# Kernel optimization log

Hardware: AMD Instinct MI355X
Metric: run time of the kernel (lower is better)

The kernel has to match this reference:

```python
import jax, jax.numpy as jnp
import numpy as np

B = 8192

def setup_inputs() -> dict:
    key = jax.random.key(0)
    k1, k2, k3 = jax.random.split(key, 3)
    pred = jax.random.normal(k1, (B,), dtype=jnp.float32)
    frac_time = jax.random.uniform(k2, (B,), dtype=jnp.float32) * 100.0
    if_mof = (jax.random.uniform(k3, (B,)) < 0.7).astype(jnp.float32)  # 0/1 flags
    gt = jnp.stack([frac_time, if_mof], axis=1)  # [B, 2]
    return {"pred": pred, "gt": gt, "gt_fracTime": 0, "gt_ifMOF": 1}


def reference(pred, gt, gt_fracTime, gt_ifMOF):
    # pred: [B], gt: [B,2]
    target = gt[:, gt_fracTime]          # [B]
    if_mof = gt[:, gt_ifMOF]             # [B], 0/1 flags
    flag = (if_mof == 1).astype(pred.dtype)
    n = pred.shape[0]
    # valid pairs: i < j with both flags set (loss term is symmetric in (i,j))
    triu = jnp.triu(jnp.ones((n, n), dtype=bool), k=1)
    pair_mask = (flag[:, None] * flag[None, :]) * triu.astype(pred.dtype)  # [B,B]
    dp = pred[:, None] - pred[None, :]      # [B,B]
    dt = target[:, None] - target[None, :]  # [B,B]
    loss = jnp.maximum(dp * dt / 100.0, 0.0)
    n_pairs = pair_mask.sum()
    return (loss * pair_mask).sum() / n_pairs
```

## Files before the change

kernel.cpp:

```cpp
#include <hip/hip_runtime.h>

#define NELEM 8192
#define JTILE 32
#define NJT   (NELEM / JTILE)
#define IPT   16
#define IBLK  (256 * IPT)
#define NIB   (NELEM / IBLK)
#define NBLK  (NIB * NJT)

__global__ __launch_bounds__(256) void pair_kernel(
    const float* __restrict__ pred,
    const float* __restrict__ gt,
    const int* __restrict__ colT,
    const int* __restrict__ colF,
    float* __restrict__ ws)
{
    __shared__ float2 sj[JTILE];
    const int tid = threadIdx.x;
    const int ib  = blockIdx.x;
    const int tj  = blockIdx.y;
    const int ct  = colT[0];
    const int cf  = colF[0];

    if (tid < JTILE) {
        const int j = tj * JTILE + tid;
        const float2 g = ((const float2*)gt)[j];
        const float tv = (ct == 0) ? g.x : g.y;
        const float fv = (cf == 0) ? g.x : g.y;
        const float pj = pred[j];
        const bool  fl = (fv == 1.0f);
        sj[tid] = make_float2(fl ? pj : 0.0f, fl ? tv * 0.01f : 0.0f);
    }
    __syncthreads();

    float p[IPT], t[IPT], f[IPT], acc[IPT];
    #pragma unroll
    for (int k = 0; k < IPT; ++k) {
        const int i = ib * IBLK + k * 256 + tid;
        const float2 g = ((const float2*)gt)[i];
        p[k] = pred[i];
        t[k] = ((ct == 0) ? g.x : g.y) * 0.01f;
        f[k] = (((cf == 0) ? g.x : g.y) == 1.0f) ? 1.0f : 0.0f;
        acc[k] = 0.0f;
    }

    #pragma unroll 4
    for (int jj = 0; jj < JTILE; ++jj) {
        const float2 v = sj[jj];
        #pragma unroll
        for (int k = 0; k < IPT; ++k)
            acc[k] = fmaf(fabsf(p[k] - v.x), fabsf(t[k] - v.y), acc[k]);
    }

    float s = 0.0f;
    #pragma unroll
    for (int k = 0; k < IPT; ++k) s = fmaf(f[k], acc[k], s);

    for (int off = 32; off > 0; off >>= 1) s += __shfl_down(s, off, 64);
    __shared__ float wsum[4];
    if ((tid & 63) == 0) wsum[tid >> 6] = s;
    __syncthreads();
    if (tid == 0) ws[tj * NIB + ib] = wsum[0] + wsum[1] + wsum[2] + wsum[3];

    if (tj == 0) {
        float c = 0, sp = 0, st = 0, spt = 0, sab = 0;
        #pragma unroll
        for (int k = 0; k < IPT; ++k) {
            const float pt = p[k] * t[k];
            c   += f[k];
            sp   = fmaf(f[k], p[k], sp);
            st   = fmaf(f[k], t[k], st);
            spt  = fmaf(f[k], pt, spt);
            sab  = fmaf(f[k], fabsf(pt), sab);
        }
        for (int off = 32; off > 0; off >>= 1) {
            c   += __shfl_down(c,   off, 64);
            sp  += __shfl_down(sp,  off, 64);
            st  += __shfl_down(st,  off, 64);
            spt += __shfl_down(spt, off, 64);
            sab += __shfl_down(sab, off, 64);
        }
        __shared__ float s5[4][5];
        const int wid = tid >> 6;
        if ((tid & 63) == 0) {
            s5[wid][0] = c;  s5[wid][1] = sp;  s5[wid][2] = st;
            s5[wid][3] = spt; s5[wid][4] = sab;
        }
        __syncthreads();
        if (tid == 0) {
            float* o = ws + NBLK + ib * 5;
            #pragma unroll
            for (int m = 0; m < 5; ++m)
                o[m] = s5[0][m] + s5[1][m] + s5[2][m] + s5[3][m];
        }
    }
}

__global__ __launch_bounds__(256) void finalize(
    const float* __restrict__ ws,
    float* __restrict__ out)
{
    const int tid = threadIdx.x;
    double s = 0.0;
    for (int i = tid; i < NBLK; i += 256) s += (double)ws[i];
    for (int off = 32; off > 0; off >>= 1) s += __shfl_down(s, off, 64);
    __shared__ double sd[4];
    if ((tid & 63) == 0) sd[tid >> 6] = s;
    __syncthreads();
    if (tid == 0) {
        const double Braw = sd[0] + sd[1] + sd[2] + sd[3];
        double M = 0, P = 0, Q = 0, T = 0, D = 0;
        for (int ib = 0; ib < NIB; ++ib) {
            const float* o = ws + NBLK + ib * 5;
            M += (double)o[0]; P += (double)o[1]; Q += (double)o[2];
            T += (double)o[3]; D += (double)o[4];
        }
        const double A = 2.0 * (M * T - P * Q);
        const double B = Braw - ((double)NELEM - M) * D;
        out[0] = (float)((A + B) / (2.0 * M * (M - 1.0)));
    }
}

extern "C" void kernel_launch(void* const* d_in, const int* in_sizes, int n_in,
                              void* d_out, int out_size, void* d_ws, size_t ws_size,
                              hipStream_t stream) {
    const float* pred = (const float*)d_in[0];
    const float* gt   = (const float*)d_in[1];
    const int*   colT = (const int*)d_in[2];
    const int*   colF = (const int*)d_in[3];

    float* ws = (float*)d_ws;

    dim3 grid(NIB, NJT);
    pair_kernel<<<grid, 256, 0, stream>>>(pred, gt, colT, colF, ws);
    finalize<<<1, 256, 0, stream>>>(ws, (float*)d_out);
}
```

Measured before the change: 16.61 us.

## Fuse finalize into pair kernel via last-block atomic counter; halve IPT

Merges the separate finalize kernel into the pair kernel. Each block writes its partial sums with atomic stores and bumps a global counter, and whichever block arrives last performs the double-precision final reduction. It also halves the rows each thread handles, which doubles the block count for better CU coverage, and fully unrolls the inner j loop. A hipMemsetAsync is added to reset the counter, so a memset replaces the second kernel launch rather than removing a launch entirely.

```diff
diff --git a/kernel.cpp b/kernel.cpp
--- a/kernel.cpp
+++ b/kernel.cpp
@@ -3,19 +3,26 @@
 #define NELEM 8192
 #define JTILE 32
 #define NJT   (NELEM / JTILE)
-#define IPT   16
+#define IPT   8
 #define IBLK  (256 * IPT)
 #define NIB   (NELEM / IBLK)
 #define NBLK  (NIB * NJT)
+#define SCB   NBLK
 
-__global__ __launch_bounds__(256) void pair_kernel(
+__global__ __launch_bounds__(256) void cindex_fused(
     const float* __restrict__ pred,
     const float* __restrict__ gt,
     const int* __restrict__ colT,
     const int* __restrict__ colF,
-    float* __restrict__ ws)
+    float* __restrict__ ws,
+    unsigned int* __restrict__ counter,
+    float* __restrict__ out)
 {
     __shared__ float2 sj[JTILE];
+    __shared__ float  wsum[4];
+    __shared__ float  s5[4][5];
+    __shared__ int    lastBlock;
+
     const int tid = threadIdx.x;
     const int ib  = blockIdx.x;
     const int tj  = blockIdx.y;
@@ -44,7 +51,7 @@
         acc[k] = 0.0f;
     }
 
-    #pragma unroll 4
+    #pragma unroll
     for (int jj = 0; jj < JTILE; ++jj) {
         const float2 v = sj[jj];
         #pragma unroll
@@ -55,12 +62,8 @@
     float s = 0.0f;
     #pragma unroll
     for (int k = 0; k < IPT; ++k) s = fmaf(f[k], acc[k], s);
-
     for (int off = 32; off > 0; off >>= 1) s += __shfl_down(s, off, 64);
-    __shared__ float wsum[4];
     if ((tid & 63) == 0) wsum[tid >> 6] = s;
-    __syncthreads();
-    if (tid == 0) ws[tj * NIB + ib] = wsum[0] + wsum[1] + wsum[2] + wsum[3];
 
     if (tj == 0) {
         float c = 0, sp = 0, st = 0, spt = 0, sab = 0;
@@ -80,40 +83,50 @@
             spt += __shfl_down(spt, off, 64);
             sab += __shfl_down(sab, off, 64);
         }
-        __shared__ float s5[4][5];
-        const int wid = tid >> 6;
         if ((tid & 63) == 0) {
-            s5[wid][0] = c;  s5[wid][1] = sp;  s5[wid][2] = st;
-            s5[wid][3] = spt; s5[wid][4] = sab;
+            const int w = tid >> 6;
+            s5[w][0] = c;  s5[w][1] = sp;  s5[w][2] = st;
+            s5[w][3] = spt; s5[w][4] = sab;
         }
-        __syncthreads();
-        if (tid == 0) {
-            float* o = ws + NBLK + ib * 5;
+    }
+    __syncthreads();
+
+    if (tid == 0) {
+        const float bsum = wsum[0] + wsum[1] + wsum[2] + wsum[3];
+        __hip_atomic_store(&ws[tj * NIB + ib], bsum,
+                           __ATOMIC_RELAXED, __HIP_MEMORY_SCOPE_AGENT);
+        if (tj == 0) {
             #pragma unroll
             for (int m = 0; m < 5; ++m)
-                o[m] = s5[0][m] + s5[1][m] + s5[2][m] + s5[3][m];
+                __hip_atomic_store(&ws[SCB + ib * 5 + m],
+                                   s5[0][m] + s5[1][m] + s5[2][m] + s5[3][m],
+                                   __ATOMIC_RELAXED, __HIP_MEMORY_SCOPE_AGENT);
         }
+        const unsigned old = __hip_atomic_fetch_add(counter, 1u,
+                                __ATOMIC_ACQ_REL, __HIP_MEMORY_SCOPE_AGENT);
+        lastBlock = (old == NBLK - 1) ? 1 : 0;
     }
-}
+    __syncthreads();
+    if (!lastBlock) return;
 
-__global__ __launch_bounds__(256) void finalize(
-    const float* __restrict__ ws,
-    float* __restrict__ out)
-{
-    const int tid = threadIdx.x;
-    double s = 0.0;
-    for (int i = tid; i < NBLK; i += 256) s += (double)ws[i];
-    for (int off = 32; off > 0; off >>= 1) s += __shfl_down(s, off, 64);
+    double d = 0.0;
+    for (int i = tid; i < NBLK; i += 256)
+        d += (double)__hip_atomic_load(&ws[i],
+                        __ATOMIC_RELAXED, __HIP_MEMORY_SCOPE_AGENT);
+    for (int off = 32; off > 0; off >>= 1) d += __shfl_down(d, off, 64);
     __shared__ double sd[4];
-    if ((tid & 63) == 0) sd[tid >> 6] = s;
+    if ((tid & 63) == 0) sd[tid >> 6] = d;
     __syncthreads();
     if (tid == 0) {
         const double Braw = sd[0] + sd[1] + sd[2] + sd[3];
         double M = 0, P = 0, Q = 0, T = 0, D = 0;
-        for (int ib = 0; ib < NIB; ++ib) {
-            const float* o = ws + NBLK + ib * 5;
-            M += (double)o[0]; P += (double)o[1]; Q += (double)o[2];
-            T += (double)o[3]; D += (double)o[4];
+        for (int ibb = 0; ibb < NIB; ++ibb) {
+            const float* o = ws + SCB + ibb * 5;
+            M += (double)__hip_atomic_load(&o[0], __ATOMIC_RELAXED, __HIP_MEMORY_SCOPE_AGENT);
+            P += (double)__hip_atomic_load(&o[1], __ATOMIC_RELAXED, __HIP_MEMORY_SCOPE_AGENT);
+            Q += (double)__hip_atomic_load(&o[2], __ATOMIC_RELAXED, __HIP_MEMORY_SCOPE_AGENT);
+            T += (double)__hip_atomic_load(&o[3], __ATOMIC_RELAXED, __HIP_MEMORY_SCOPE_AGENT);
+            D += (double)__hip_atomic_load(&o[4], __ATOMIC_RELAXED, __HIP_MEMORY_SCOPE_AGENT);
         }
         const double A = 2.0 * (M * T - P * Q);
         const double B = Braw - ((double)NELEM - M) * D;
@@ -130,8 +143,10 @@
     const int*   colF = (const int*)d_in[3];
 
     float* ws = (float*)d_ws;
+    unsigned int* counter = (unsigned int*)(ws + 2048);
 
+    hipMemsetAsync(counter, 0, sizeof(unsigned int), stream);
     dim3 grid(NIB, NJT);
-    pair_kernel<<<grid, 256, 0, stream>>>(pred, gt, colT, colF, ws);
-    finalize<<<1, 256, 0, stream>>>(ws, (float*)d_out);
+    cindex_fused<<<grid, 256, 0, stream>>>(pred, gt, colT, colF, ws,
+                                           counter, (float*)d_out);
 }
```

Measured after the change: 32.70 us. 1.97x slower.
